# Kernel tuning notes

Measured on AMD Instinct MI355X. Metric: run time of the kernel, lower is better.

## Reference

```python
import jax, jax.numpy as jnp
import numpy as np

N_FFT = 200; HOP = 100; N_FREQ = N_FFT // 2 + 1  # 101
EMB = 256; HEADS = 8; DHEAD = EMB // HEADS; DEPTH = 4
N_CH = 23; B = 256; TS = 2000
MASK_RATIO = 0.9


def _layernorm(x, s, b):
    mu = jnp.mean(x, -1, keepdims=True)
    var = jnp.mean((x - mu) ** 2, -1, keepdims=True)
    return (x - mu) * jax.lax.rsqrt(var + 1e-5) * s + b


def _posenc(T, d):
    pos = jnp.arange(T, dtype=jnp.float32)[:, None]
    div = jnp.exp(jnp.arange(0, d, 2, dtype=jnp.float32) * (-np.log(10000.0) / d))
    pe = jnp.zeros((T, d), jnp.float32)
    pe = pe.at[:, 0::2].set(jnp.sin(pos * div))
    pe = pe.at[:, 1::2].set(jnp.cos(pos * div))
    return pe


def setup_inputs() -> dict:
    key = jax.random.key(0)
    ks = jax.random.split(key, 12)
    def n(k, shape):
        return (jax.random.normal(k, shape) * 0.02).astype(jnp.float32)
    T = 1 + (TS - N_FFT) // HOP  # 19
    S = N_CH * T                 # 437
    return dict(
        x=jax.random.normal(ks[0], (B, N_CH, TS), jnp.float32),
        mask_noise=jax.random.uniform(ks[1], (B, S, EMB), dtype=jnp.float32),
        W_proj=n(ks[2], (N_FREQ, EMB)), b_proj=jnp.zeros((EMB,), jnp.float32),
        channel_tokens=n(ks[3], (N_CH, EMB)),
        ln1_s=jnp.ones((DEPTH, EMB), jnp.float32), ln1_b=jnp.zeros((DEPTH, EMB), jnp.float32),
        Wq=n(ks[4], (DEPTH, EMB, EMB)), Wk=n(ks[5], (DEPTH, EMB, EMB)),
        Wv=n(ks[6], (DEPTH, EMB, EMB)), Wo=n(ks[7], (DEPTH, EMB, EMB)),
        bo=jnp.zeros((DEPTH, EMB), jnp.float32),
        ln2_s=jnp.ones((DEPTH, EMB), jnp.float32), ln2_b=jnp.zeros((DEPTH, EMB), jnp.float32),
        W1=n(ks[8], (DEPTH, EMB, 4 * EMB)), b1=jnp.zeros((DEPTH, 4 * EMB), jnp.float32),
        W2=n(ks[9], (DEPTH, 4 * EMB, EMB)), b2=jnp.zeros((DEPTH, EMB), jnp.float32),
    )


def _forward(x, mask_noise, W_proj, b_proj, channel_tokens,
             ln1_s, ln1_b, Wq, Wk, Wv, Wo, bo, ln2_s, ln2_b, W1, b1, W2, b2):
    Bb, C, ts = x.shape
    T = 1 + (ts - N_FFT) // HOP
    # ---- vectorized per-channel STFT (rect window, center=False, onesided) ----
    idx = jnp.arange(T)[:, None] * HOP + jnp.arange(N_FFT)[None, :]  # [T, n_fft]
    frames = x[:, :, idx]                                            # [B,C,T,n_fft]
    spec = jnp.abs(jnp.fft.rfft(frames, axis=-1)).astype(x.dtype)    # [B,C,T,F]
    # patch embedding (Linear over freq), channel token, positional encoding
    emb = spec @ W_proj + b_proj                                     # [B,C,T,E]
    emb = emb + channel_tokens[:C][None, :, None, :]
    emb = emb + _posenc(T, emb.shape[-1])[None, None]
    emb = emb.reshape(Bb, C * T, -1)                                 # [B,S,E]
    # ---- random masking (mask_ratio=0.9 as hard-coded in forward) ----
    mask = mask_noise < MASK_RATIO
    masked = jnp.where(mask, jnp.zeros((), emb.dtype), emb)
    # ---- LinearAttentionTransformer (non-causal linear attention, pre-norm) ----
    h = masked
    for l in range(DEPTH):
        y = _layernorm(h, ln1_s[l], ln1_b[l])
        S = y.shape[1]
        q = (y @ Wq[l]).reshape(Bb, S, HEADS, DHEAD).transpose(0, 2, 1, 3)
        k = (y @ Wk[l]).reshape(Bb, S, HEADS, DHEAD).transpose(0, 2, 1, 3)
        v = (y @ Wv[l]).reshape(Bb, S, HEADS, DHEAD).transpose(0, 2, 1, 3)
        q = jax.nn.softmax(q, axis=-1) * (DHEAD ** -0.5)
        k = jax.nn.softmax(k, axis=2)  # softmax over sequence
        ctx = jnp.einsum('bhnd,bhne->bhde', k, v)     # [B,H,d,d] global context
        att = jnp.einsum('bhnd,bhde->bhne', q, ctx)   # [B,H,S,d]
        att = att.transpose(0, 2, 1, 3).reshape(Bb, S, EMB)
        h = h + att @ Wo[l] + bo[l]
        y = _layernorm(h, ln2_s[l], ln2_b[l])
        h = h + jax.nn.gelu(y @ W1[l] + b1[l]) @ W2[l] + b2[l]
    return emb, masked, h, mask


def reference(x, mask_noise, W_proj, b_proj, channel_tokens,
              ln1_s, ln1_b, Wq, Wk, Wv, Wo, bo, ln2_s, ln2_b, W1, b1, W2, b2):
    return _forward(x, mask_noise, W_proj, b_proj, channel_tokens,
                    ln1_s, ln1_b, Wq, Wk, Wv, Wo, bo, ln2_s, ln2_b, W1, b1, W2, b2)
```

## Files before the change

kernel.cpp:

```cpp
#include <hip/hip_runtime.h>

#define BB    256
#define NCH   23
#define TT    19
#define SS    437
#define BSR   111872
#define EMBD  256
#define NHEAD 8
#define DH    32
#define NFREQ 101
#define NFFT  200
#define HOPSZ 100
#define TSLEN 2000
#define HID   1024
#define NDEPTH 4
#define NTOK  28639232
#define QKVW  768
#define WL    786432
#define CDL   3584

typedef __attribute__((ext_vector_type(8))) __bf16 bf16x8;
typedef __attribute__((ext_vector_type(8))) unsigned short u16x8;
typedef __attribute__((ext_vector_type(4))) float  f32x4;

__device__ __forceinline__ float gelu_f(float x){
    return 0.5f*x*(1.0f + tanhf(0.7978845608028654f*(x + 0.044715f*x*x*x)));
}
__device__ __forceinline__ unsigned short f2b(float f){
    unsigned u = __float_as_uint(f);
    return (unsigned short)((u + 0x7FFFu + ((u >> 16) & 1u)) >> 16);
}
__device__ __forceinline__ float b2f(unsigned short h){
    return __uint_as_float(((unsigned)h) << 16);
}

__device__ __forceinline__ void swz_tile(int& bx, int& by){
    int nx = gridDim.x, nwg = nx * gridDim.y;
    int lid = blockIdx.y * nx + blockIdx.x;
    int q = nwg >> 3, r = nwg & 7;
    int xcd = lid & 7, off = lid >> 3;
    int wgid = (xcd < r ? xcd*(q+1) : r*(q+1) + (xcd-r)*q) + off;
    bx = wgid % nx; by = wgid / nx;
}

__global__ void init_twb(unsigned short* __restrict__ tw){
    int i = blockIdx.x*256 + threadIdx.x;
    if(i >= 256*256) return;
    int n = i >> 8, k = i & 255;
    float v = 0.f;
    if(k < NFFT && n < 2*NFREQ){
        int f = n >> 1;
        int ph = (f * k) % NFFT;
        float ang = 6.283185307179586f * (float)ph / (float)NFFT;
        v = (n & 1) ? sinf(ang) : cosf(ang);
    }
    tw[i] = f2b(v);
}

__global__ void init_pe(float* __restrict__ pe){
    int i = blockIdx.x*256 + threadIdx.x;
    if(i >= TT*EMBD) return;
    int t = i / EMBD, e = i % EMBD;
    int j = e >> 1;
    float div = expf((float)(2*j) * (-9.210340371976184f/256.0f));
    float ang = (float)t * div;
    pe[i] = (e & 1) ? cosf(ang) : sinf(ang);
}

__global__ void wprep_proj(const float* __restrict__ Wp, unsigned short* __restrict__ Wt){
    int i = blockIdx.x*256 + threadIdx.x;
    if(i >= 256*128) return;
    int e = i >> 7, k = i & 127;
    Wt[i] = f2b(k < NFREQ ? Wp[(size_t)k*EMBD + e] : 0.f);
}

__global__ void wprep_qkv(const float* __restrict__ Wq, const float* __restrict__ Wk,
                          const float* __restrict__ Wv, const float* __restrict__ ln1s,
                          unsigned short* __restrict__ wbuf){
    long i = (long)blockIdx.x*256 + threadIdx.x;
    if(i >= (long)NDEPTH*QKVW*EMBD) return;
    int l = (int)(i / (QKVW*EMBD));
    int rem = (int)(i % (QKVW*EMBD));
    int n = rem >> 8, k = rem & 255;
    const float* W = (n < 256) ? Wq : (n < 512) ? Wk : Wv;
    float s = ln1s[l*EMBD + k];
    wbuf[(size_t)l*WL + rem] = f2b(s * W[(size_t)l*65536 + (size_t)k*256 + (n & 255)]);
}
__global__ void wprep_wo(const float* __restrict__ Wo, unsigned short* __restrict__ wbuf){
    int i = blockIdx.x*256 + threadIdx.x;
    if(i >= NDEPTH*65536) return;
    int l = i >> 16, rem = i & 65535;
    int n = rem >> 8, k = rem & 255;
    wbuf[(size_t)l*WL + 196608 + rem] = f2b(Wo[(size_t)l*65536 + (size_t)k*256 + n]);
}
__global__ void wprep_w1(const float* __restrict__ W1, const float* __restrict__ ln2s,
                         unsigned short* __restrict__ wbuf){
    long i = (long)blockIdx.x*256 + threadIdx.x;
    if(i >= (long)NDEPTH*262144) return;
    int l = (int)(i >> 18), rem = (int)(i & 262143);
    int n = rem >> 8, k = rem & 255;
    float s = ln2s[l*EMBD + k];
    wbuf[(size_t)l*WL + 262144 + rem] = f2b(s * W1[(size_t)l*262144 + (size_t)k*1024 + n]);
}
__global__ void wprep_w2(const float* __restrict__ W2, unsigned short* __restrict__ wbuf){
    long i = (long)blockIdx.x*256 + threadIdx.x;
    if(i >= (long)NDEPTH*262144) return;
    int l = (int)(i >> 18), rem = (int)(i & 262143);
    int n = rem >> 10, k = rem & 1023;
    wbuf[(size_t)l*WL + 524288 + rem] = f2b(W2[(size_t)l*262144 + (size_t)k*256 + n]);
}

__global__ void prep_cd(const float* __restrict__ Wq, const float* __restrict__ Wk,
                        const float* __restrict__ Wv, const float* __restrict__ W1,
                        const float* __restrict__ ln1s, const float* __restrict__ ln1b,
                        const float* __restrict__ ln2s, const float* __restrict__ ln2b,
                        const float* __restrict__ b1, float* __restrict__ cd){
    int i = blockIdx.x*256 + threadIdx.x;
    if(i >= NDEPTH*1792) return;
    int l = i / 1792, r = i % 1792;
    float c = 0.f, d = 0.f;
    if(r < 768){
        const float* W = (r < 256) ? Wq : (r < 512) ? Wk : Wv;
        int n = r & 255;
        for(int k = 0; k < 256; ++k){
            float w = W[(size_t)l*65536 + (size_t)k*256 + n];
            c = fmaf(ln1s[l*EMBD+k], w, c);
            d = fmaf(ln1b[l*EMBD+k], w, d);
        }
        cd[(size_t)l*CDL + r]       = c;
        cd[(size_t)l*CDL + 768 + r] = d;
    } else {
        int n = r - 768;
        for(int k = 0; k < 256; ++k){
            float w = W1[(size_t)l*262144 + (size_t)k*1024 + n];
            c = fmaf(ln2s[l*EMBD+k], w, c);
            d = fmaf(ln2b[l*EMBD+k], w, d);
        }
        cd[(size_t)l*CDL + 1536 + n] = c;
        cd[(size_t)l*CDL + 2560 + n] = d + b1[l*HID + n];
    }
}

#define GEMM_CORE(A_, B_, K_) \
    f32x4 acc[4][4]; \
    _Pragma("unroll") \
    for(int i=0;i<4;++i) \
        _Pragma("unroll") \
        for(int jj=0;jj<4;++jj) acc[i][jj] = (f32x4){0.f,0.f,0.f,0.f}; \
    const int srow0 = w*32 + (l>>3); \
    const int sgrp  = l & 7; \
    for(int k0 = 0; k0 < (K_); k0 += 64){ \
        _Pragma("unroll") \
        for(int it=0; it<4; ++it){ \
            int row  = srow0 + it*8; \
            int colA = ((sgrp ^ (row & 7)) << 3); \
            const unsigned short* ga = (A_) + (size_t)(m0+row)*(K_) + k0 + colA; \
            const unsigned short* gb = (B_) + (size_t)(n0+row)*(K_) + k0 + colA; \
            __builtin_amdgcn_global_load_lds( \
                (__attribute__((address_space(1))) void*)ga, \
                (__attribute__((address_space(3))) void*)(As + w*2048 + it*512), \
                16, 0, 0); \
            __builtin_amdgcn_global_load_lds( \
                (__attribute__((address_space(1))) void*)gb, \
                (__attribute__((address_space(3))) void*)(Bs + w*2048 + it*512), \
                16, 0, 0); \
        } \
        __syncthreads(); \
        GEMM_MFMA_PHASE \
        __syncthreads(); \
    }

#define GEMM_MFMA_PHASE \
        _Pragma("unroll") \
        for(int kk=0; kk<2; ++kk){ \
            bf16x8 af[4], bfr[4]; \
            _Pragma("unroll") \
            for(int mi=0;mi<4;++mi){ \
                int row = wr*64 + mi*16 + (l & 15); \
                int grp = kk*4 + (l >> 4); \
                af[mi] = *(const bf16x8*)&As[row*64 + ((grp ^ (row&7))<<3)]; \
            } \
            _Pragma("unroll") \
            for(int ni=0;ni<4;++ni){ \
                int row = wc*64 + ni*16 + (l & 15); \
                int grp = kk*4 + (l >> 4); \
                bfr[ni] = *(const bf16x8*)&Bs[row*64 + ((grp ^ (row&7))<<3)]; \
            } \
            _Pragma("unroll") \
            for(int mi=0;mi<4;++mi) \
                _Pragma("unroll") \
                for(int ni=0;ni<4;++ni) \
                    acc[mi][ni] = __builtin_amdgcn_mfma_f32_16x16x32_bf16( \
                        af[mi], bfr[ni], acc[mi][ni], 0, 0, 0); \
        }

template<int MODE>
__global__ __launch_bounds__(256) void gemm_mfma(
    const unsigned short* __restrict__ A, const unsigned short* __restrict__ Bt,
    const float* __restrict__ bias, void* __restrict__ Cv,
    const unsigned short* __restrict__ Cin, int M, int N, int K)
{
    __shared__ __align__(16) unsigned short As[128*64];
    __shared__ __align__(16) unsigned short Bs[128*64];
    const int tid = threadIdx.x;
    const int w = tid >> 6, l = tid & 63;
    int bx, by; swz_tile(bx, by);
    const int m0 = by * 128, n0 = bx * 128;
    const int wr = w >> 1, wc = w & 1;
    GEMM_CORE(A, Bt, K)
    const int cn  = l & 15;
    const int cr4 = (l >> 4) * 4;
    #pragma unroll
    for(int ni=0;ni<4;++ni){
        int n = n0 + wc*64 + ni*16 + cn;
        float bn = bias[n];
        #pragma unroll
        for(int mi=0;mi<4;++mi){
            int mB = m0 + wr*64 + mi*16 + cr4;
            #pragma unroll
            for(int r=0;r<4;++r){
                size_t off = (size_t)(mB+r)*N + n;
                float v = acc[mi][ni][r];
                if(MODE == 1)
                    ((unsigned short*)Cv)[off] = f2b(b2f(Cin[off]) + v + bn);
                else
                    ((float*)Cv)[off] = b2f(Cin[off]) + v + bn;
            }
        }
    }
}

template<int GELU>
__global__ __launch_bounds__(256, 4) void gemm_ln(
    const unsigned short* __restrict__ A, const unsigned short* __restrict__ Bt,
    void* __restrict__ Cv,
    const float* __restrict__ muv, const float* __restrict__ rsv,
    const float* __restrict__ cvec, const float* __restrict__ dvec,
    int M, int N, int K)
{
    __shared__ __align__(16) unsigned short As[128*64];
    __shared__ __align__(16) unsigned short Bs[128*64];
    const int tid = threadIdx.x;
    const int w = tid >> 6, l = tid & 63;
    int bx, by; swz_tile(bx, by);
    const int m0 = by * 128, n0 = bx * 128;
    const int wr = w >> 1, wc = w & 1;
    GEMM_CORE(A, Bt, K)
    const int cn  = l & 15;
    const int cr4 = (l >> 4) * 4;
    float cv[4], dv[4];
    #pragma unroll
    for(int ni=0;ni<4;++ni){
        int n = n0 + wc*64 + ni*16 + cn;
        cv[ni] = cvec[n]; dv[ni] = dvec[n];
    }
    #pragma unroll
    for(int mi=0;mi<4;++mi){
        #pragma unroll
        for(int r=0;r<4;++r){
            int m = m0 + wr*64 + mi*16 + cr4 + r;
            float mu = muv[m], rs = rsv[m];
            float c0 = rs * mu;
            #pragma unroll
            for(int ni=0;ni<4;++ni){
                int n = n0 + wc*64 + ni*16 + cn;
                float y = rs*acc[mi][ni][r] - c0*cv[ni] + dv[ni];
                ((unsigned short*)Cv)[(size_t)m*N + n] = f2b(GELU ? gelu_f(y) : y);
            }
        }
    }
}

__global__ __launch_bounds__(256) void gemm_dft(
    const float* __restrict__ x, const unsigned short* __restrict__ Bt,
    unsigned short* __restrict__ spec)
{
    const int K = 256;
    __shared__ __align__(16) unsigned short As[128*64];
    __shared__ __align__(16) unsigned short Bs[128*64];
    const int tid = threadIdx.x;
    const int w = tid >> 6, l = tid & 63;
    int bx, by; swz_tile(bx, by);
    const int m0 = by * 128, n0 = bx * 128;
    const int wr = w >> 1, wc = w & 1;
    f32x4 acc[4][4];
    #pragma unroll
    for(int i=0;i<4;++i)
        #pragma unroll
        for(int jj=0;jj<4;++jj) acc[i][jj] = (f32x4){0.f,0.f,0.f,0.f};
    const int sgrp = l & 7;
    for(int k0 = 0; k0 < K; k0 += 64){
        #pragma unroll
        for(int it=0; it<4; ++it){
            int row = w*32 + it*8 + (l>>3);
            int kg  = sgrp ^ (row & 7);
            int kb  = k0 + kg*8;
            int m   = m0 + row;
            int t   = m % TT;
            long bc = m / TT;
            const float* src = x + bc*(long)TSLEN + (long)t*HOPSZ + kb;
            u16x8 v;
            #pragma unroll
            for(int j=0;j<8;++j){
                float f = (kb + j < NFFT) ? src[j] : 0.f;
                v[j] = f2b(f);
            }
            *(u16x8*)&As[row*64 + sgrp*8] = v;
            int colB = (kg << 3);
            const unsigned short* gb = Bt + (size_t)(n0+row)*K + k0 + colB;
            __builtin_amdgcn_global_load_lds(
                (__attribute__((address_space(1))) void*)gb,
                (__attribute__((address_space(3))) void*)(Bs + w*2048 + it*512),
                16, 0, 0);
        }
        __syncthreads();
        GEMM_MFMA_PHASE
        __syncthreads();
    }
    const int cn  = l & 15;
    const int cr4 = (l >> 4) * 4;
    #pragma unroll
    for(int ni=0;ni<4;++ni){
        int n = n0 + wc*64 + ni*16 + cn;
        #pragma unroll
        for(int mi=0;mi<4;++mi){
            int mB = m0 + wr*64 + mi*16 + cr4;
            #pragma unroll
            for(int r=0;r<4;++r){
                float own = acc[mi][ni][r];
                float par = __shfl_xor(own, 1, 64);
                if(!(cn & 1)){
                    float sv = sqrtf(own*own + par*par);
                    spec[(size_t)(mB+r)*128 + (n >> 1)] = f2b(sv);
                }
            }
        }
    }
}

__global__ __launch_bounds__(256) void gemm_emb(
    const unsigned short* __restrict__ A, const unsigned short* __restrict__ Bt,
    const float* __restrict__ bp, const float* __restrict__ ctok,
    const float* __restrict__ pe, const float* __restrict__ noise,
    float* __restrict__ o_emb, float* __restrict__ o_masked,
    float* __restrict__ o_mask, unsigned short* __restrict__ bufH)
{
    const int K = 128, N = 256;
    __shared__ __align__(16) unsigned short As[128*64];
    __shared__ __align__(16) unsigned short Bs[128*64];
    const int tid = threadIdx.x;
    const int w = tid >> 6, l = tid & 63;
    int bx, by; swz_tile(bx, by);
    const int m0 = by * 128, n0 = bx * 128;
    const int wr = w >> 1, wc = w & 1;
    GEMM_CORE(A, Bt, K)
    const int cn  = l & 15;
    const int cr4 = (l >> 4) * 4;
    #pragma unroll
    for(int ni=0;ni<4;++ni){
        int n = n0 + wc*64 + ni*16 + cn;
        float bn = bp[n];
        #pragma unroll
        for(int mi=0;mi<4;++mi){
            int mB = m0 + wr*64 + mi*16 + cr4;
            #pragma unroll
            for(int r=0;r<4;++r){
                int m = mB + r;
                int t = m % TT;
                int c = (m / TT) % NCH;
                size_t off = (size_t)m*EMBD + n;
                float v = acc[mi][ni][r] + bn + ctok[c*EMBD + n] + pe[t*EMBD + n];
                o_emb[off] = v;
                float mn = noise[off];
                bool  msk = mn < 0.9f;
                float md = msk ? 0.f : v;
                bufH[off]     = f2b(md);
                o_masked[off] = md;
                o_mask[off]   = msk ? 1.f : 0.f;
            }
        }
    }
}

__global__ __launch_bounds__(256) void row_stats(const unsigned short* __restrict__ X,
    float* __restrict__ muv, float* __restrict__ rsv)
{
    int w = threadIdx.x >> 6, lane = threadIdx.x & 63;
    long row = (long)blockIdx.x*4 + w;
    ushort4 u = *(const ushort4*)(X + row*EMBD + lane*4);
    float x0 = b2f(u.x), x1 = b2f(u.y), x2 = b2f(u.z), x3 = b2f(u.w);
    float sum = x0 + x1 + x2 + x3;
    #pragma unroll
    for(int o=32;o>0;o>>=1) sum += __shfl_xor(sum, o, 64);
    float mu = sum * (1.0f/256.0f);
    float dx = x0-mu, dy = x1-mu, dz = x2-mu, dw = x3-mu;
    float vs = dx*dx + dy*dy + dz*dz + dw*dw;
    #pragma unroll
    for(int o=32;o>0;o>>=1) vs += __shfl_xor(vs, o, 64);
    if(lane == 0){
        muv[row] = mu;
        rsv[row] = rsqrtf(vs*(1.0f/256.0f) + 1e-5f);
    }
}

__global__ __launch_bounds__(256) void ctx_kernel(const unsigned short* __restrict__ qkvb,
    float* __restrict__ ctx)
{
    __shared__ float kt[16][DH], vt[16][DH];
    __shared__ float sm[8][32], ss[8][32];
    __shared__ float kmsL[32], kinvL[32];
    int bh = blockIdx.x; int b = bh >> 3, h = bh & 7;
    int tid = threadIdx.x;
    {
        int d = tid & 31, g = tid >> 5;
        const unsigned short* p = qkvb + (size_t)b*SS*QKVW + 256 + h*DH + d;
        float m = -1e30f, s = 0.f;
        for(int n = g; n < SS; n += 8){
            float xv = b2f(p[(size_t)n*QKVW]);
            if(xv > m){ s = s*expf(m-xv) + 1.f; m = xv; }
            else      { s += expf(xv-m); }
        }
        sm[g][d] = m; ss[g][d] = s;
    }
    __syncthreads();
    if(tid < 32){
        float M = sm[0][tid], S = ss[0][tid];
        #pragma unroll
        for(int o = 1; o < 8; ++o){
            float m2 = sm[o][tid], s2 = ss[o][tid];
            if(m2 > M){ S = S*expf(M-m2) + s2; M = m2; }
            else      { S += s2*expf(m2-M); }
        }
        kmsL[tid] = M; kinvL[tid] = 1.0f / S;
    }
    __syncthreads();
    int d = tid >> 3, e4 = (tid & 7) * 4;
    float km = kmsL[d];
    float a0=0,a1=0,a2=0,a3=0;
    for(int n0=0;n0<SS;n0+=16){
        __syncthreads();
        #pragma unroll
        for(int i=0;i<2;++i){
            int e = tid + i*256;
            int nn = e >> 5, dd = e & 31;
            int n = n0 + nn;
            float kv, vv;
            if(n < SS){
                size_t off = ((size_t)(b*SS+n))*QKVW + h*DH + dd;
                kv = b2f(qkvb[off + 256]);
                vv = b2f(qkvb[off + 512]);
            } else { kv = -1e30f; vv = 0.f; }
            kt[nn][dd] = kv; vt[nn][dd] = vv;
        }
        __syncthreads();
        #pragma unroll
        for(int nn=0;nn<16;++nn){
            float ke = expf(kt[nn][d] - km);
            a0 = fmaf(ke, vt[nn][e4+0], a0);
            a1 = fmaf(ke, vt[nn][e4+1], a1);
            a2 = fmaf(ke, vt[nn][e4+2], a2);
            a3 = fmaf(ke, vt[nn][e4+3], a3);
        }
    }
    float inv = kinvL[d];
    float* op = ctx + ((size_t)bh*DH + d)*DH + e4;
    op[0]=a0*inv; op[1]=a1*inv; op[2]=a2*inv; op[3]=a3*inv;
}

__global__ __launch_bounds__(256) void att_kernel(const unsigned short* __restrict__ qkvb,
    const float* __restrict__ ctx, unsigned short* __restrict__ att)
{
    __shared__ float qs[4][EMBD];
    int w = threadIdx.x >> 6, lane = threadIdx.x & 63;
    int b = blockIdx.y;
    int s = blockIdx.x*4 + w;
    if(s >= SS) return;
    long row = (long)b*SS + s;
    ushort4 qu = *(const ushort4*)(qkvb + (size_t)row*QKVW + lane*4);
    float4 q4 = make_float4(b2f(qu.x), b2f(qu.y), b2f(qu.z), b2f(qu.w));
    float m = fmaxf(fmaxf(q4.x,q4.y), fmaxf(q4.z,q4.w));
    #pragma unroll
    for(int o=1;o<8;o<<=1) m = fmaxf(m, __shfl_xor(m, o, 64));
    float e0 = expf(q4.x-m), e1 = expf(q4.y-m), e2 = expf(q4.z-m), e3 = expf(q4.w-m);
    float ssum = e0+e1+e2+e3;
    #pragma unroll
    for(int o=1;o<8;o<<=1) ssum += __shfl_xor(ssum, o, 64);
    float sc = 0.17677669529663687f / ssum;
    *(float4*)&qs[w][lane*4] = make_float4(e0*sc, e1*sc, e2*sc, e3*sc);
    int head = lane >> 3;
    int ecol = (lane & 7) * 4;
    const float* cb = ctx + ((size_t)(b*NHEAD + head))*DH*DH + ecol;
    float a0=0,a1=0,a2=0,a3=0;
    #pragma unroll
    for(int d=0; d<DH; ++d){
        float qd = qs[w][head*DH + d];
        float4 c4 = *(const float4*)(cb + d*DH);
        a0 = fmaf(qd, c4.x, a0);
        a1 = fmaf(qd, c4.y, a1);
        a2 = fmaf(qd, c4.z, a2);
        a3 = fmaf(qd, c4.w, a3);
    }
    ushort4 o4; o4.x=f2b(a0); o4.y=f2b(a1); o4.z=f2b(a2); o4.w=f2b(a3);
    *(ushort4*)(att + row*EMBD + lane*4) = o4;
}

extern "C" void kernel_launch(void* const* d_in, const int* in_sizes, int n_in,
                              void* d_out, int out_size, void* d_ws, size_t ws_size,
                              hipStream_t stream)
{
    if(n_in != 18) return;

    const float* x     = (const float*)d_in[0];
    const float* noise = (const float*)d_in[1];
    const float* Wproj = (const float*)d_in[2];
    const float* bproj = (const float*)d_in[3];
    const float* ctok  = (const float*)d_in[4];
    const float* ln1s  = (const float*)d_in[5];
    const float* ln1b  = (const float*)d_in[6];
    const float* Wq    = (const float*)d_in[7];
    const float* Wk    = (const float*)d_in[8];
    const float* Wv    = (const float*)d_in[9];
    const float* Wo    = (const float*)d_in[10];
    const float* bo    = (const float*)d_in[11];
    const float* ln2s  = (const float*)d_in[12];
    const float* ln2b  = (const float*)d_in[13];
    const float* W1    = (const float*)d_in[14];
    const float* b1    = (const float*)d_in[15];
    const float* W2    = (const float*)d_in[16];
    const float* b2    = (const float*)d_in[17];

    char* p = (char*)d_ws;
    unsigned short* bufHb = (unsigned short*)p;           p += (size_t)NTOK*2;
    float* big = (float*)p;                               p += (size_t)NTOK*2*4;
    unsigned short* qkvb   = (unsigned short*)big;
    unsigned short* hidb   = (unsigned short*)big;
    unsigned short* specb  = (unsigned short*)p;          p += (size_t)BSR*128*2;
    unsigned short* attb   = (unsigned short*)p;          p += (size_t)NTOK*2;
    float* muv  = (float*)p;                              p += (size_t)BSR*4;
    float* rsv  = (float*)p;                              p += (size_t)BSR*4;
    float* cdb  = (float*)p;                              p += (size_t)NDEPTH*CDL*4;
    float* ctxb = (float*)p;                              p += (size_t)BB*NHEAD*DH*DH*4;
    float* peb  = (float*)p;                              p += (size_t)TT*EMBD*4;
    unsigned short* twb  = (unsigned short*)p;            p += (size_t)65536*2;
    unsigned short* Wpb  = (unsigned short*)p;            p += (size_t)32768*2;
    unsigned short* wbuf = (unsigned short*)p;            p += (size_t)4*WL*2;
    if(ws_size < (size_t)(p - (char*)d_ws)) return;

    float* out      = (float*)d_out;
    float* o_emb    = out;
    float* o_masked = out + (size_t)NTOK;
    float* o_h      = out + 2*(size_t)NTOK;
    float* o_mask   = out + 3*(size_t)NTOK;

    dim3 blk(256);

    init_twb<<<256, blk, 0, stream>>>(twb);
    init_pe <<<19,  blk, 0, stream>>>(peb);
    wprep_proj<<<128, blk, 0, stream>>>(Wproj, Wpb);
    wprep_qkv<<<3072, blk, 0, stream>>>(Wq, Wk, Wv, ln1s, wbuf);
    wprep_wo <<<1024, blk, 0, stream>>>(Wo, wbuf);
    wprep_w1 <<<4096, blk, 0, stream>>>(W1, ln2s, wbuf);
    wprep_w2 <<<4096, blk, 0, stream>>>(W2, wbuf);
    prep_cd  <<<28,   blk, 0, stream>>>(Wq, Wk, Wv, W1, ln1s, ln1b, ln2s, ln2b, b1, cdb);

    gemm_dft<<<dim3(2,874), blk, 0, stream>>>(x, twb, specb);
    gemm_emb<<<dim3(2,874), blk, 0, stream>>>(specb, Wpb, bproj, ctok, peb, noise,
                                              o_emb, o_masked, o_mask, bufHb);

    for(int l=0;l<NDEPTH;++l){
        unsigned short* wl   = wbuf + (size_t)l*WL;
        unsigned short* Wqkv = wl;
        unsigned short* Wot  = wl + 196608;
        unsigned short* W1t  = wl + 262144;
        unsigned short* W2t  = wl + 524288;
        float* cq = cdb + (size_t)l*CDL;
        float* dq = cq + 768;
        float* c1 = cq + 1536;
        float* d1 = cq + 2560;

        row_stats<<<BSR/4, blk, 0, stream>>>(bufHb, muv, rsv);
        gemm_ln<0><<<dim3(6,874), blk, 0, stream>>>(bufHb, Wqkv, qkvb,
                                    muv, rsv, cq, dq, BSR, QKVW, EMBD);
        ctx_kernel<<<BB*NHEAD, blk, 0, stream>>>(qkvb, ctxb);
        att_kernel<<<dim3(110, BB), blk, 0, stream>>>(qkvb, ctxb, attb);
        gemm_mfma<1><<<dim3(2,874), blk, 0, stream>>>(attb, Wot, bo + l*EMBD, bufHb,
                                    bufHb, BSR, EMBD, EMBD);
        row_stats<<<BSR/4, blk, 0, stream>>>(bufHb, muv, rsv);
        gemm_ln<1><<<dim3(8,874), blk, 0, stream>>>(bufHb, W1t, hidb,
                                    muv, rsv, c1, d1, BSR, HID, EMBD);
        if(l == NDEPTH-1)
            gemm_mfma<4><<<dim3(2,874), blk, 0, stream>>>(hidb, W2t, b2 + l*EMBD, o_h,
                                    bufHb, BSR, EMBD, HID);
        else
            gemm_mfma<1><<<dim3(2,874), blk, 0, stream>>>(hidb, W2t, b2 + l*EMBD, bufHb,
                                    bufHb, BSR, EMBD, HID);
    }
}
```

Baseline: 3.136 ms.

## Fuse LayerNorm row statistics into GEMM epilogues via atomic partial sums

Removes the separate row_stats kernels. The residual-writing GEMM epilogues (embedding and output/FFN projections) now accumulate per-row sum and sum-of-squares, reduce them through shuffles and LDS, and atomically add them into a zeroed buffer. The LN-folded GEMMs then derive mean and rstd as E[x²]−μ². This saves one full read pass over the activations per LayerNorm, at the cost of memsets, atomics, a less stable variance formula, and stats taken from fp32 values rather than the stored bf16 values. Launch bounds for gemm_mfma also gain a minimum-occupancy hint.

```diff
diff --git a/kernel.cpp b/kernel.cpp
--- a/kernel.cpp
+++ b/kernel.cpp
@@ -194,11 +194,22 @@
                         af[mi], bfr[ni], acc[mi][ni], 0, 0, 0); \
         }
 
-template<int MODE>
-__global__ __launch_bounds__(256) void gemm_mfma(
+#define STATS_REDUCE_STORE(rb_, s1_, s2_) \
+    { \
+        _Pragma("unroll") \
+        for(int o=1;o<16;o<<=1){ s1_ += __shfl_xor(s1_, o, 64); s2_ += __shfl_xor(s2_, o, 64); } \
+        if(cn == 0){ \
+            slds[((rb_)*2 + wc)*2 + 0] = s1_; \
+            slds[((rb_)*2 + wc)*2 + 1] = s2_; \
+        } \
+    }
+
+template<int MODE, int STATS>
+__global__ __launch_bounds__(256, 4) void gemm_mfma(
     const unsigned short* __restrict__ A, const unsigned short* __restrict__ Bt,
     const float* __restrict__ bias, void* __restrict__ Cv,
-    const unsigned short* __restrict__ Cin, int M, int N, int K)
+    const unsigned short* __restrict__ Cin, float* __restrict__ sums,
+    int M, int N, int K)
 {
     __shared__ __align__(16) unsigned short As[128*64];
     __shared__ __align__(16) unsigned short Bs[128*64];
@@ -210,22 +221,36 @@
     GEMM_CORE(A, Bt, K)
     const int cn  = l & 15;
     const int cr4 = (l >> 4) * 4;
-    #pragma unroll
-    for(int ni=0;ni<4;++ni){
-        int n = n0 + wc*64 + ni*16 + cn;
-        float bn = bias[n];
-        #pragma unroll
-        for(int mi=0;mi<4;++mi){
-            int mB = m0 + wr*64 + mi*16 + cr4;
+    float* slds = (float*)As;
+    float bnv[4];
+    #pragma unroll
+    for(int ni=0;ni<4;++ni) bnv[ni] = bias[n0 + wc*64 + ni*16 + cn];
+    #pragma unroll
+    for(int mi=0;mi<4;++mi){
+        #pragma unroll
+        for(int r=0;r<4;++r){
+            int rb = wr*64 + mi*16 + cr4 + r;
+            int m  = m0 + rb;
+            float s1 = 0.f, s2 = 0.f;
             #pragma unroll
-            for(int r=0;r<4;++r){
-                size_t off = (size_t)(mB+r)*N + n;
-                float v = acc[mi][ni][r];
-                if(MODE == 1)
-                    ((unsigned short*)Cv)[off] = f2b(b2f(Cin[off]) + v + bn);
-                else
-                    ((float*)Cv)[off] = b2f(Cin[off]) + v + bn;
+            for(int ni=0;ni<4;++ni){
+                int n = n0 + wc*64 + ni*16 + cn;
+                size_t off = (size_t)m*N + n;
+                float v = b2f(Cin[off]) + acc[mi][ni][r] + bnv[ni];
+                if(MODE == 1) ((unsigned short*)Cv)[off] = f2b(v);
+                else          ((float*)Cv)[off] = v;
+                if(STATS){ s1 += v; s2 += v*v; }
             }
+            if(STATS) STATS_REDUCE_STORE(rb, s1, s2)
+        }
+    }
+    if(STATS){
+        __syncthreads();
+        if(tid < 128){
+            float t1 = slds[(tid*2+0)*2+0] + slds[(tid*2+1)*2+0];
+            float t2 = slds[(tid*2+0)*2+1] + slds[(tid*2+1)*2+1];
+            atomicAdd(&sums[(size_t)(m0+tid)*2],   t1);
+            atomicAdd(&sums[(size_t)(m0+tid)*2+1], t2);
         }
     }
 }
@@ -233,8 +258,7 @@
 template<int GELU>
 __global__ __launch_bounds__(256, 4) void gemm_ln(
     const unsigned short* __restrict__ A, const unsigned short* __restrict__ Bt,
-    void* __restrict__ Cv,
-    const float* __restrict__ muv, const float* __restrict__ rsv,
+    void* __restrict__ Cv, const float* __restrict__ sums,
     const float* __restrict__ cvec, const float* __restrict__ dvec,
     int M, int N, int K)
 {
@@ -259,7 +283,9 @@
         #pragma unroll
         for(int r=0;r<4;++r){
             int m = m0 + wr*64 + mi*16 + cr4 + r;
-            float mu = muv[m], rs = rsv[m];
+            float mu  = sums[(size_t)m*2]   * (1.0f/256.0f);
+            float ex2 = sums[(size_t)m*2+1] * (1.0f/256.0f);
+            float rs = rsqrtf(ex2 - mu*mu + 1e-5f);
             float c0 = rs * mu;
             #pragma unroll
             for(int ni=0;ni<4;++ni){
@@ -343,7 +369,8 @@
     const float* __restrict__ bp, const float* __restrict__ ctok,
     const float* __restrict__ pe, const float* __restrict__ noise,
     float* __restrict__ o_emb, float* __restrict__ o_masked,
-    float* __restrict__ o_mask, unsigned short* __restrict__ bufH)
+    float* __restrict__ o_mask, unsigned short* __restrict__ bufH,
+    float* __restrict__ sums)
 {
     const int K = 128, N = 256;
     __shared__ __align__(16) unsigned short As[128*64];
@@ -356,20 +383,24 @@
     GEMM_CORE(A, Bt, K)
     const int cn  = l & 15;
     const int cr4 = (l >> 4) * 4;
-    #pragma unroll
-    for(int ni=0;ni<4;++ni){
-        int n = n0 + wc*64 + ni*16 + cn;
-        float bn = bp[n];
-        #pragma unroll
-        for(int mi=0;mi<4;++mi){
-            int mB = m0 + wr*64 + mi*16 + cr4;
+    float* slds = (float*)As;
+    float bnv[4];
+    #pragma unroll
+    for(int ni=0;ni<4;++ni) bnv[ni] = bp[n0 + wc*64 + ni*16 + cn];
+    #pragma unroll
+    for(int mi=0;mi<4;++mi){
+        #pragma unroll
+        for(int r=0;r<4;++r){
+            int rb = wr*64 + mi*16 + cr4 + r;
+            int m  = m0 + rb;
+            int t = m % TT;
+            int c = (m / TT) % NCH;
+            float s1 = 0.f, s2 = 0.f;
             #pragma unroll
-            for(int r=0;r<4;++r){
-                int m = mB + r;
-                int t = m % TT;
-                int c = (m / TT) % NCH;
+            for(int ni=0;ni<4;++ni){
+                int n = n0 + wc*64 + ni*16 + cn;
                 size_t off = (size_t)m*EMBD + n;
-                float v = acc[mi][ni][r] + bn + ctok[c*EMBD + n] + pe[t*EMBD + n];
+                float v = acc[mi][ni][r] + bnv[ni] + ctok[c*EMBD + n] + pe[t*EMBD + n];
                 o_emb[off] = v;
                 float mn = noise[off];
                 bool  msk = mn < 0.9f;
@@ -377,29 +408,17 @@
                 bufH[off]     = f2b(md);
                 o_masked[off] = md;
                 o_mask[off]   = msk ? 1.f : 0.f;
+                s1 += md; s2 += md*md;
             }
-        }
-    }
-}
-
-__global__ __launch_bounds__(256) void row_stats(const unsigned short* __restrict__ X,
-    float* __restrict__ muv, float* __restrict__ rsv)
-{
-    int w = threadIdx.x >> 6, lane = threadIdx.x & 63;
-    long row = (long)blockIdx.x*4 + w;
-    ushort4 u = *(const ushort4*)(X + row*EMBD + lane*4);
-    float x0 = b2f(u.x), x1 = b2f(u.y), x2 = b2f(u.z), x3 = b2f(u.w);
-    float sum = x0 + x1 + x2 + x3;
-    #pragma unroll
-    for(int o=32;o>0;o>>=1) sum += __shfl_xor(sum, o, 64);
-    float mu = sum * (1.0f/256.0f);
-    float dx = x0-mu, dy = x1-mu, dz = x2-mu, dw = x3-mu;
-    float vs = dx*dx + dy*dy + dz*dz + dw*dw;
-    #pragma unroll
-    for(int o=32;o>0;o>>=1) vs += __shfl_xor(vs, o, 64);
-    if(lane == 0){
-        muv[row] = mu;
-        rsv[row] = rsqrtf(vs*(1.0f/256.0f) + 1e-5f);
+            STATS_REDUCE_STORE(rb, s1, s2)
+        }
+    }
+    __syncthreads();
+    if(tid < 128){
+        float t1 = slds[(tid*2+0)*2+0] + slds[(tid*2+1)*2+0];
+        float t2 = slds[(tid*2+0)*2+1] + slds[(tid*2+1)*2+1];
+        atomicAdd(&sums[(size_t)(m0+tid)*2],   t1);
+        atomicAdd(&sums[(size_t)(m0+tid)*2+1], t2);
     }
 }
 
@@ -536,8 +555,8 @@
     unsigned short* hidb   = (unsigned short*)big;
     unsigned short* specb  = (unsigned short*)p;          p += (size_t)BSR*128*2;
     unsigned short* attb   = (unsigned short*)p;          p += (size_t)NTOK*2;
-    float* muv  = (float*)p;                              p += (size_t)BSR*4;
-    float* rsv  = (float*)p;                              p += (size_t)BSR*4;
+    float* sums1 = (float*)p;                             p += (size_t)BSR*2*4;
+    float* sums2 = (float*)p;                             p += (size_t)BSR*2*4;
     float* cdb  = (float*)p;                              p += (size_t)NDEPTH*CDL*4;
     float* ctxb = (float*)p;                              p += (size_t)BB*NHEAD*DH*DH*4;
     float* peb  = (float*)p;                              p += (size_t)TT*EMBD*4;
@@ -553,6 +572,7 @@
     float* o_mask   = out + 3*(size_t)NTOK;
 
     dim3 blk(256);
+    const size_t SB = (size_t)BSR*2*4;
 
     init_twb<<<256, blk, 0, stream>>>(twb);
     init_pe <<<19,  blk, 0, stream>>>(peb);
@@ -563,9 +583,10 @@
     wprep_w2 <<<4096, blk, 0, stream>>>(W2, wbuf);
     prep_cd  <<<28,   blk, 0, stream>>>(Wq, Wk, Wv, W1, ln1s, ln1b, ln2s, ln2b, b1, cdb);
 
+    hipMemsetAsync(sums1, 0, SB, stream);
     gemm_dft<<<dim3(2,874), blk, 0, stream>>>(x, twb, specb);
     gemm_emb<<<dim3(2,874), blk, 0, stream>>>(specb, Wpb, bproj, ctok, peb, noise,
-                                              o_emb, o_masked, o_mask, bufHb);
+                                              o_emb, o_masked, o_mask, bufHb, sums1);
 
     for(int l=0;l<NDEPTH;++l){
         unsigned short* wl   = wbuf + (size_t)l*WL;
@@ -578,21 +599,22 @@
         float* c1 = cq + 1536;
         float* d1 = cq + 2560;
 
-        row_stats<<<BSR/4, blk, 0, stream>>>(bufHb, muv, rsv);
         gemm_ln<0><<<dim3(6,874), blk, 0, stream>>>(bufHb, Wqkv, qkvb,
-                                    muv, rsv, cq, dq, BSR, QKVW, EMBD);
+                                    sums1, cq, dq, BSR, QKVW, EMBD);
         ctx_kernel<<<BB*NHEAD, blk, 0, stream>>>(qkvb, ctxb);
         att_kernel<<<dim3(110, BB), blk, 0, stream>>>(qkvb, ctxb, attb);
-        gemm_mfma<1><<<dim3(2,874), blk, 0, stream>>>(attb, Wot, bo + l*EMBD, bufHb,
-                                    bufHb, BSR, EMBD, EMBD);
-        row_stats<<<BSR/4, blk, 0, stream>>>(bufHb, muv, rsv);
+        hipMemsetAsync(sums2, 0, SB, stream);
+        gemm_mfma<1,1><<<dim3(2,874), blk, 0, stream>>>(attb, Wot, bo + l*EMBD, bufHb,
+                                    bufHb, sums2, BSR, EMBD, EMBD);
         gemm_ln<1><<<dim3(8,874), blk, 0, stream>>>(bufHb, W1t, hidb,
-                                    muv, rsv, c1, d1, BSR, HID, EMBD);
-        if(l == NDEPTH-1)
-            gemm_mfma<4><<<dim3(2,874), blk, 0, stream>>>(hidb, W2t, b2 + l*EMBD, o_h,
-                                    bufHb, BSR, EMBD, HID);
-        else
-            gemm_mfma<1><<<dim3(2,874), blk, 0, stream>>>(hidb, W2t, b2 + l*EMBD, bufHb,
-                                    bufHb, BSR, EMBD, HID);
-    }
-}
+                                    sums2, c1, d1, BSR, HID, EMBD);
+        if(l == NDEPTH-1){
+            gemm_mfma<4,0><<<dim3(2,874), blk, 0, stream>>>(hidb, W2t, b2 + l*EMBD, o_h,
+                                    bufHb, nullptr, BSR, EMBD, HID);
+        } else {
+            hipMemsetAsync(sums1, 0, SB, stream);
+            gemm_mfma<1,1><<<dim3(2,874), blk, 0, stream>>>(hidb, W2t, b2 + l*EMBD, bufHb,
+                                    bufHb, sums1, BSR, EMBD, HID);
+        }
+    }
+}
```

Result: faster. 2.961 ms, median of 2 (-5.6%).
